# Kernel optimization log

Measured on AMD Instinct MI355X. Metric: run time of the kernel, lower is better.

The kernel has to match this reference:

```python
import jax, jax.numpy as jnp
import numpy as np

BS, T, S_LEN = 128, 256, 40
NV, NS = 2048, 300
VH, SH = 512, 512
L_CROSS, N_LOC, N_FEAT = 512, 128, 1024


def _linear_params(key, out_d, in_d):
    k1, k2 = jax.random.split(key)
    lim = 1.0 / np.sqrt(in_d)
    W = jax.random.uniform(k1, (out_d, in_d), jnp.float32, -lim, lim)
    b = jax.random.uniform(k2, (out_d,), jnp.float32, -lim, lim)
    return W, b


def setup_inputs() -> dict:
    key = jax.random.key(0)
    ks = jax.random.split(key, 12)
    gv = jax.random.normal(ks[0], (BS, T, NV), jnp.float32)
    sen = jax.random.normal(ks[1], (BS, S_LEN, NS), jnp.float32)
    visual_fea = jax.random.normal(ks[2], (BS, T, 2 * VH), jnp.float32)
    sen_fea = jax.random.normal(ks[3], (BS, 2 * SH), jnp.float32)
    loc = jax.random.uniform(ks[4], (BS, 2), jnp.float32)  # normalized start/end in [0,1)
    v_len = jax.random.randint(ks[5], (BS,), 1, T + 1)
    video_mask = (jnp.arange(T)[None, :] < v_len[:, None]).astype(jnp.int32)
    s_len = jax.random.randint(ks[6], (BS,), 1, S_LEN + 1)
    sen_mask = (jnp.arange(S_LEN)[None, :] < s_len[:, None]).astype(jnp.int32)
    W1, b1 = _linear_params(ks[7], L_CROSS, 2 * VH)
    W2, b2 = _linear_params(ks[8], L_CROSS, 2 * SH)
    W3, b3 = _linear_params(ks[9], N_LOC, 2)
    n_cat = 2 * (VH + SH) + L_CROSS + N_LOC
    W4, b4 = _linear_params(ks[10], N_FEAT, n_cat)
    return dict(step=1, gv=gv, sen=sen, visual_fea=visual_fea, sen_fea=sen_fea,
                loc=loc, sen_mask=sen_mask, video_mask=video_mask,
                W1=W1, b1=b1, W2=W2, b2=b2, W3=W3, b3=b3, W4=W4, b4=b4)


def _pool_and_head(visual_fea, sen_fea, loc, video_mask,
                   W1, b1, W2, b2, W3, b3, W4, b4):
    dt = visual_fea.dtype
    n_frame = visual_fea.shape[1]
    v_len = video_mask.sum(1)  # [B] int
    valid = (jnp.arange(n_frame)[None, :] < v_len[:, None]).astype(dt)  # [B,T]
    # global mean over valid frames
    gv_fea = (visual_fea * valid[:, :, None]).sum(1) / v_len[:, None].astype(dt)
    # local mean over [start, end] with start/end = floor(loc * (len-1)) (torch int() trunc, loc>=0)
    idx = jnp.floor(loc * (v_len[:, None] - 1).astype(loc.dtype)).astype(jnp.int32)
    s, e = idx[:, 0], idx[:, 1]
    csum = jnp.cumsum(visual_fea, axis=1)
    csum = jnp.concatenate([jnp.zeros_like(csum[:, :1]), csum], axis=1)  # [B,T+1,D]
    seg_sum = (jnp.take_along_axis(csum, (e + 1)[:, None, None], axis=1)
               - jnp.take_along_axis(csum, s[:, None, None], axis=1))[:, 0, :]
    cnt = jnp.maximum(e + 1 - s, 1).astype(dt)
    lv_fea = jnp.where((s <= e)[:, None], seg_sum / cnt[:, None], jnp.zeros((), dt))
    # fused head
    vs = jax.nn.relu((lv_fea @ W1.T + b1) * (sen_fea @ W2.T + b2))
    loc_fea = jax.nn.relu(loc @ W3.T + b3)
    out = jnp.concatenate([sen_fea, gv_fea, vs, loc_fea], axis=1)
    feature = jax.nn.relu(out @ W4.T + b4)
    return feature


def reference(step, gv, sen, visual_fea, sen_fea, loc, sen_mask, video_mask,
              W1, b1, W2, b2, W3, b3, W4, b4):
    # step != 0 hot path: GRU encodes (step==0 one-time branch) are skipped;
    # visual_fea / sen_fea are carried over from the step-0 call, as in the original.
    assert step != 0, 'reference covers the recurrent hot path (step > 0)'
    feature = _pool_and_head(visual_fea, sen_fea, loc, video_mask,
                             W1, b1, W2, b2, W3, b3, W4, b4)
    return visual_fea, sen_fea, feature
```

## Files before the change

### kernel.cpp

```cpp
#include <hip/hip_runtime.h>

#define BS 128
#define T 256
#define D 1024
#define NCAT 2688
#define NLOC 128
#define NFEAT 1024

typedef short bf16x8 __attribute__((ext_vector_type(8)));
typedef float f32x4 __attribute__((ext_vector_type(4)));
typedef unsigned short u16;
typedef u16 u16x4 __attribute__((ext_vector_type(4)));

__device__ __forceinline__ u16 f2bf(float f) {
    unsigned int u = __float_as_uint(f);
    u += 0x7fffu + ((u >> 16) & 1u);
    return (u16)(u >> 16);
}

__global__ void ka_copy_pool_w(const float* __restrict__ vf, float* __restrict__ out0,
                               const int* __restrict__ vmask, const float* __restrict__ loc,
                               const float* __restrict__ W1, const float* __restrict__ W2,
                               const float* __restrict__ W4,
                               u16* __restrict__ W1b, u16* __restrict__ W2b,
                               u16* __restrict__ W4b,
                               float* __restrict__ pgv, float* __restrict__ pseg) {
    int blk = blockIdx.x, tid = threadIdx.x;

    if (blk >= 1024) {
        int i = (blk - 1024) * 256 + tid;
        const float* src; u16* dst;
        if (i < 131072)      { src = W1 + 4 * i;            dst = W1b + 4 * i; }
        else if (i < 262144) { src = W2 + 4 * (i - 131072); dst = W2b + 4 * (i - 131072); }
        else                 { src = W4 + 4 * (i - 262144); dst = W4b + 4 * (i - 262144); }
        f32x4 v = *(const f32x4*)src;
        u16x4 o;
#pragma unroll
        for (int j = 0; j < 4; ++j) o[j] = f2bf(v[j]);
        *(u16x4*)dst = o;
        return;
    }

    int b = blk >> 3, tc = blk & 7;
    __shared__ int red[256];
    __shared__ int sse[3];
    red[tid] = vmask[b * T + tid];
    __syncthreads();
    for (int off = 128; off > 0; off >>= 1) {
        if (tid < off) red[tid] += red[tid + off];
        __syncthreads();
    }
    if (tid == 0) {
        int vl = red[0];
        float sc = (float)(vl - 1);
        sse[0] = vl;
        sse[1] = (int)floorf(loc[2 * b] * sc);
        sse[2] = (int)floorf(loc[2 * b + 1] * sc);
    }
    __syncthreads();
    int vl = sse[0], s = sse[1], e = sse[2];

    int d0 = tid * 4;
    f32x4 g  = {0.f, 0.f, 0.f, 0.f};
    f32x4 sg = {0.f, 0.f, 0.f, 0.f};
    const float* src = vf   + ((size_t)(b * T + tc * 32)) * D + d0;
    float*       dst = out0 + ((size_t)(b * T + tc * 32)) * D + d0;

    for (int i = 0; i < 32; ++i) {
        f32x4 v = *(const f32x4*)src;
        __builtin_nontemporal_store(v, (f32x4*)dst);
        int t = tc * 32 + i;
        if (t < vl) g += v;
        if (t >= s && t <= e) sg += v;
        src += D; dst += D;
    }
    int o = (b * 8 + tc) * D + d0;
    *(f32x4*)(pgv  + o) = g;
    *(f32x4*)(pseg + o) = sg;
}

__global__ void k2_build(const float* __restrict__ sen_fea, const float* __restrict__ loc,
                         const float* __restrict__ W3, const float* __restrict__ b3,
                         const int* __restrict__ vmask,
                         const float* __restrict__ pgv, const float* __restrict__ pseg,
                         u16* __restrict__ lv_bf, u16* __restrict__ cat,
                         float* __restrict__ out1) {
    int b = blockIdx.x, tid = threadIdx.x;
    __shared__ int red[256];
    __shared__ int sse[3];
    red[tid] = vmask[b * T + tid];
    __syncthreads();
    for (int off = 128; off > 0; off >>= 1) {
        if (tid < off) red[tid] += red[tid + off];
        __syncthreads();
    }
    if (tid == 0) {
        int vl = red[0];
        float sc = (float)(vl - 1);
        sse[0] = vl;
        sse[1] = (int)floorf(loc[2 * b] * sc);
        sse[2] = (int)floorf(loc[2 * b + 1] * sc);
    }
    __syncthreads();
    int vl = sse[0], s = sse[1], e = sse[2];

    float inv_vl = 1.0f / (float)vl;
    int cnt = e + 1 - s; if (cnt < 1) cnt = 1;
    float inv_cnt = 1.0f / (float)cnt;
    bool valid = (s <= e);

    for (int d = tid; d < D; d += 256) {
        float gs = 0.f, ss = 0.f;
#pragma unroll
        for (int c = 0; c < 8; ++c) {
            gs += pgv [(b * 8 + c) * D + d];
            ss += pseg[(b * 8 + c) * D + d];
        }
        cat[b * NCAT + 1024 + d] = f2bf(gs * inv_vl);
        lv_bf[b * D + d] = f2bf(valid ? ss * inv_cnt : 0.f);
        float sf = sen_fea[b * D + d];
        cat[b * NCAT + d] = f2bf(sf);
        out1[b * D + d] = sf;
    }
    if (tid < NLOC) {
        float v = loc[2 * b] * W3[2 * tid] + loc[2 * b + 1] * W3[2 * tid + 1] + b3[tid];
        cat[b * NCAT + 2560 + tid] = f2bf(fmaxf(v, 0.f));
    }
}

__global__ void k3_vs(const u16* __restrict__ lv, const u16* __restrict__ cat_ro,
                      const u16* __restrict__ W1b, const float* __restrict__ b1,
                      const u16* __restrict__ W2b, const float* __restrict__ b2,
                      u16* __restrict__ cat) {
    int wid = threadIdx.x >> 6, lane = threadIdx.x & 63;
    int mt = blockIdx.x >> 5, nt = blockIdx.x & 31;
    int m0 = mt * 16, n0 = nt * 16;
    int row = lane & 15, kg = lane >> 4;

    const u16* pa = (wid == 0) ? (lv + (m0 + row) * D + kg * 8)
                               : (cat_ro + (m0 + row) * NCAT + kg * 8);
    const u16* pb = ((wid == 0) ? W1b : W2b) + (n0 + row) * D + kg * 8;

    f32x4 acc = {0.f, 0.f, 0.f, 0.f};
    for (int k = 0; k < 1024; k += 32)
        acc = __builtin_amdgcn_mfma_f32_16x16x32_bf16(*(const bf16x8*)(pa + k),
                                                      *(const bf16x8*)(pb + k), acc, 0, 0, 0);

    int col = lane & 15, rbase = (lane >> 4) * 4;
    float bb = ((wid == 0) ? b1 : b2)[n0 + col];

    __shared__ float qs[4][64];
    if (wid == 1) {
#pragma unroll
        for (int r = 0; r < 4; ++r) qs[r][lane] = acc[r] + bb;
    }
    __syncthreads();
    if (wid == 0) {
#pragma unroll
        for (int r = 0; r < 4; ++r) {
            float p = acc[r] + bb;
            cat[(m0 + rbase + r) * NCAT + 2048 + n0 + col] = f2bf(fmaxf(p * qs[r][lane], 0.f));
        }
    }
}

__global__ void k4_feat(const u16* __restrict__ cat, const u16* __restrict__ W4b,
                        const float* __restrict__ b4, float* __restrict__ out2) {
    int wid = threadIdx.x >> 6, lane = threadIdx.x & 63;
    int mt = blockIdx.x >> 6, nt = blockIdx.x & 63;
    int m0 = mt * 16, n0 = nt * 16;
    int row = lane & 15, kg = lane >> 4;

    const u16* pa = cat + (m0 + row) * NCAT + wid * 1344 + kg * 8;
    const u16* pb = W4b + (n0 + row) * NCAT + wid * 1344 + kg * 8;

    f32x4 acc = {0.f, 0.f, 0.f, 0.f};
    for (int k = 0; k < 1344; k += 32)
        acc = __builtin_amdgcn_mfma_f32_16x16x32_bf16(*(const bf16x8*)(pa + k),
                                                      *(const bf16x8*)(pb + k), acc, 0, 0, 0);

    int col = lane & 15, rbase = (lane >> 4) * 4;
    __shared__ float qs[4][64];
    if (wid == 1) {
#pragma unroll
        for (int r = 0; r < 4; ++r) qs[r][lane] = acc[r];
    }
    __syncthreads();
    if (wid == 0) {
        float bb = b4[n0 + col];
#pragma unroll
        for (int r = 0; r < 4; ++r)
            out2[(m0 + rbase + r) * NFEAT + n0 + col] = fmaxf(acc[r] + qs[r][lane] + bb, 0.f);
    }
}

extern "C" void kernel_launch(void* const* d_in, const int* in_sizes, int n_in,
                              void* d_out, int out_size, void* d_ws, size_t ws_size,
                              hipStream_t stream) {
    (void)in_sizes; (void)n_in; (void)out_size; (void)ws_size;
    const float* vf      = (const float*)d_in[3];
    const float* sen_fea = (const float*)d_in[4];
    const float* loc     = (const float*)d_in[5];
    const int*   vmask   = (const int*)d_in[7];
    const float* W1 = (const float*)d_in[8];
    const float* b1 = (const float*)d_in[9];
    const float* W2 = (const float*)d_in[10];
    const float* b2 = (const float*)d_in[11];
    const float* W3 = (const float*)d_in[12];
    const float* b3 = (const float*)d_in[13];
    const float* W4 = (const float*)d_in[14];
    const float* b4 = (const float*)d_in[15];

    float* out0 = (float*)d_out;
    float* out1 = out0 + (size_t)BS * T * D;
    float* out2 = out1 + (size_t)BS * D;

    char* w = (char*)d_ws;
    float* pgv  = (float*)(w);
    float* pseg = (float*)(w + 4194304);
    u16*   cat  = (u16*)  (w + 2 * 4194304);
    u16*   lv   = (u16*)  (w + 2 * 4194304 + 688128);
    u16*   W1b  = (u16*)  (w + 2 * 4194304 + 950272);
    u16*   W2b  = (u16*)  (w + 2 * 4194304 + 950272 + 1048576);
    u16*   W4b  = (u16*)  (w + 2 * 4194304 + 950272 + 2097152);

    ka_copy_pool_w<<<4736, 256, 0, stream>>>(vf, out0, vmask, loc, W1, W2, W4,
                                             W1b, W2b, W4b, pgv, pseg);
    k2_build<<<BS, 256, 0, stream>>>(sen_fea, loc, W3, b3, vmask, pgv, pseg, lv, cat, out1);
    k3_vs<<<256, 128, 0, stream>>>(lv, cat, W1b, b1, W2b, b2, cat);
    k4_feat<<<512, 128, 0, stream>>>(cat, W4b, b4, out2);
}
```

Before: 71.08 us.

## Fuse pooling finalize via last-block atomic, defer padded-frame copy to overlap final GEMM

The pool kernel now reads and copies only the valid frames per batch and skips chunks past the video length. The last chunk block to finish, found with an atomic counter, does the reduction and builds the concat buffer, which removes the separate build kernel. Copying the padded frames into the output moves into the final GEMM launch so it runs alongside the MFMA work. The final GEMM also splits K across four waves instead of two. This adds a memset, an atomic counter and cross-block coordination through memory ordering.

```diff
diff --git a/kernel.cpp b/kernel.cpp
--- a/kernel.cpp
+++ b/kernel.cpp
@@ -4,7 +4,6 @@
 #define T 256
 #define D 1024
 #define NCAT 2688
-#define NLOC 128
 #define NFEAT 1024
 
 typedef short bf16x8 __attribute__((ext_vector_type(8)));
@@ -18,13 +17,18 @@
     return (u16)(u >> 16);
 }
 
-__global__ void ka_copy_pool_w(const float* __restrict__ vf, float* __restrict__ out0,
-                               const int* __restrict__ vmask, const float* __restrict__ loc,
-                               const float* __restrict__ W1, const float* __restrict__ W2,
-                               const float* __restrict__ W4,
-                               u16* __restrict__ W1b, u16* __restrict__ W2b,
-                               u16* __restrict__ W4b,
-                               float* __restrict__ pgv, float* __restrict__ pseg) {
+
+__global__ __launch_bounds__(256, 4)
+void kL1(const float* __restrict__ vf, float* __restrict__ out0,
+         const int* __restrict__ vmask, const float* __restrict__ loc,
+         const float* __restrict__ sen_fea,
+         const float* __restrict__ W1, const float* __restrict__ W2,
+         const float* __restrict__ W3, const float* __restrict__ W4,
+         const float* __restrict__ b3,
+         u16* __restrict__ W1b, u16* __restrict__ W2b, u16* __restrict__ W4b,
+         float* __restrict__ pgv, float* __restrict__ pseg,
+         u16* __restrict__ cat, u16* __restrict__ lv,
+         float* __restrict__ out1, int* __restrict__ ctl) {
     int blk = blockIdx.x, tid = threadIdx.x;
 
     if (blk >= 1024) {
@@ -44,6 +48,7 @@
     int b = blk >> 3, tc = blk & 7;
     __shared__ int red[256];
     __shared__ int sse[3];
+    __shared__ int lastf;
     red[tid] = vmask[b * T + tid];
     __syncthreads();
     for (int off = 128; off > 0; off >>= 1) {
@@ -59,73 +64,58 @@
     }
     __syncthreads();
     int vl = sse[0], s = sse[1], e = sse[2];
-
+    int nchunk = (vl + 31) >> 5;
+    if (tc >= nchunk) return;
+
+    int t0 = tc * 32;
+    int nrows = vl - t0; if (nrows > 32) nrows = 32;
     int d0 = tid * 4;
     f32x4 g  = {0.f, 0.f, 0.f, 0.f};
     f32x4 sg = {0.f, 0.f, 0.f, 0.f};
-    const float* src = vf   + ((size_t)(b * T + tc * 32)) * D + d0;
-    float*       dst = out0 + ((size_t)(b * T + tc * 32)) * D + d0;
-
-    for (int i = 0; i < 32; ++i) {
+    const float* src = vf   + ((size_t)(b * T + t0)) * D + d0;
+    float*       dst = out0 + ((size_t)(b * T + t0)) * D + d0;
+    for (int i = 0; i < nrows; ++i) {
         f32x4 v = *(const f32x4*)src;
         __builtin_nontemporal_store(v, (f32x4*)dst);
-        int t = tc * 32 + i;
-        if (t < vl) g += v;
+        g += v;
+        int t = t0 + i;
         if (t >= s && t <= e) sg += v;
         src += D; dst += D;
     }
     int o = (b * 8 + tc) * D + d0;
     *(f32x4*)(pgv  + o) = g;
     *(f32x4*)(pseg + o) = sg;
-}
-
-__global__ void k2_build(const float* __restrict__ sen_fea, const float* __restrict__ loc,
-                         const float* __restrict__ W3, const float* __restrict__ b3,
-                         const int* __restrict__ vmask,
-                         const float* __restrict__ pgv, const float* __restrict__ pseg,
-                         u16* __restrict__ lv_bf, u16* __restrict__ cat,
-                         float* __restrict__ out1) {
-    int b = blockIdx.x, tid = threadIdx.x;
-    __shared__ int red[256];
-    __shared__ int sse[3];
-    red[tid] = vmask[b * T + tid];
-    __syncthreads();
-    for (int off = 128; off > 0; off >>= 1) {
-        if (tid < off) red[tid] += red[tid + off];
-        __syncthreads();
-    }
+
+    __syncthreads();
     if (tid == 0) {
-        int vl = red[0];
-        float sc = (float)(vl - 1);
-        sse[0] = vl;
-        sse[1] = (int)floorf(loc[2 * b] * sc);
-        sse[2] = (int)floorf(loc[2 * b + 1] * sc);
-    }
-    __syncthreads();
-    int vl = sse[0], s = sse[1], e = sse[2];
+        int old = __hip_atomic_fetch_add(&ctl[b], 1,
+                                         __ATOMIC_ACQ_REL, __HIP_MEMORY_SCOPE_AGENT);
+        lastf = (old == nchunk - 1);
+    }
+    __syncthreads();
+    if (!lastf) return;
 
     float inv_vl = 1.0f / (float)vl;
     int cnt = e + 1 - s; if (cnt < 1) cnt = 1;
     float inv_cnt = 1.0f / (float)cnt;
     bool valid = (s <= e);
-
     for (int d = tid; d < D; d += 256) {
         float gs = 0.f, ss = 0.f;
-#pragma unroll
-        for (int c = 0; c < 8; ++c) {
+        for (int c = 0; c < nchunk; ++c) {
             gs += pgv [(b * 8 + c) * D + d];
             ss += pseg[(b * 8 + c) * D + d];
         }
         cat[b * NCAT + 1024 + d] = f2bf(gs * inv_vl);
-        lv_bf[b * D + d] = f2bf(valid ? ss * inv_cnt : 0.f);
+        lv[b * D + d] = f2bf(valid ? ss * inv_cnt : 0.f);
         float sf = sen_fea[b * D + d];
         cat[b * NCAT + d] = f2bf(sf);
         out1[b * D + d] = sf;
     }
-    if (tid < NLOC) {
+    if (tid < 128) {
         float v = loc[2 * b] * W3[2 * tid] + loc[2 * b + 1] * W3[2 * tid + 1] + b3[tid];
         cat[b * NCAT + 2560 + tid] = f2bf(fmaxf(v, 0.f));
     }
+    if (tid == 0) ctl[128 + b] = vl;
 }
 
 __global__ void k3_vs(const u16* __restrict__ lv, const u16* __restrict__ cat_ro,
@@ -164,33 +154,59 @@
     }
 }
 
-__global__ void k4_feat(const u16* __restrict__ cat, const u16* __restrict__ W4b,
-                        const float* __restrict__ b4, float* __restrict__ out2) {
-    int wid = threadIdx.x >> 6, lane = threadIdx.x & 63;
-    int mt = blockIdx.x >> 6, nt = blockIdx.x & 63;
-    int m0 = mt * 16, n0 = nt * 16;
-    int row = lane & 15, kg = lane >> 4;
-
-    const u16* pa = cat + (m0 + row) * NCAT + wid * 1344 + kg * 8;
-    const u16* pb = W4b + (n0 + row) * NCAT + wid * 1344 + kg * 8;
-
-    f32x4 acc = {0.f, 0.f, 0.f, 0.f};
-    for (int k = 0; k < 1344; k += 32)
-        acc = __builtin_amdgcn_mfma_f32_16x16x32_bf16(*(const bf16x8*)(pa + k),
-                                                      *(const bf16x8*)(pb + k), acc, 0, 0, 0);
-
-    int col = lane & 15, rbase = (lane >> 4) * 4;
-    __shared__ float qs[4][64];
-    if (wid == 1) {
-#pragma unroll
-        for (int r = 0; r < 4; ++r) qs[r][lane] = acc[r];
-    }
-    __syncthreads();
-    if (wid == 0) {
-        float bb = b4[n0 + col];
-#pragma unroll
-        for (int r = 0; r < 4; ++r)
-            out2[(m0 + rbase + r) * NFEAT + n0 + col] = fmaxf(acc[r] + qs[r][lane] + bb, 0.f);
+__global__ __launch_bounds__(256, 4)
+void kL3(const float* __restrict__ vf, float* __restrict__ out0,
+         const u16* __restrict__ cat, const u16* __restrict__ W4b,
+         const float* __restrict__ b4, float* __restrict__ out2,
+         const int* __restrict__ ctl) {
+    int blk = blockIdx.x, tid = threadIdx.x;
+    __shared__ float qsf[3][4][64];
+
+    if (blk < 512) {
+        int mt = blk >> 6, nt = blk & 63;
+        int wid = tid >> 6, lane = tid & 63;
+        int m0 = mt * 16, n0 = nt * 16;
+        int row = lane & 15, kg = lane >> 4;
+
+        const u16* pa = cat + (m0 + row) * NCAT + wid * 672 + kg * 8;
+        const u16* pb = W4b + (n0 + row) * NCAT + wid * 672 + kg * 8;
+
+        f32x4 acc = {0.f, 0.f, 0.f, 0.f};
+        for (int k = 0; k < 672; k += 32)
+            acc = __builtin_amdgcn_mfma_f32_16x16x32_bf16(*(const bf16x8*)(pa + k),
+                                                          *(const bf16x8*)(pb + k), acc, 0, 0, 0);
+        int col = lane & 15, rbase = (lane >> 4) * 4;
+        if (wid) {
+#pragma unroll
+            for (int r = 0; r < 4; ++r) qsf[wid - 1][r][lane] = acc[r];
+        }
+        __syncthreads();
+        if (wid == 0) {
+            float bb = b4[n0 + col];
+#pragma unroll
+            for (int r = 0; r < 4; ++r) {
+                float v = acc[r] + qsf[0][r][lane] + qsf[1][r][lane] + qsf[2][r][lane] + bb;
+                out2[(m0 + rbase + r) * NFEAT + n0 + col] = fmaxf(v, 0.f);
+            }
+        }
+        return;
+    }
+
+    int bi = blk - 512;
+    int b = bi >> 3, tc = bi & 7;
+    int vl = ctl[128 + b];
+    int t0 = tc * 32;
+    int start = (vl > t0) ? vl : t0;
+    int end = t0 + 32;
+    if (start >= end) return;
+
+    int d0 = tid * 4;
+    const float* src = vf   + ((size_t)(b * T + start)) * D + d0;
+    float*       dst = out0 + ((size_t)(b * T + start)) * D + d0;
+    for (int t = start; t < end; ++t) {
+        f32x4 v = *(const f32x4*)src;
+        __builtin_nontemporal_store(v, (f32x4*)dst);
+        src += D; dst += D;
     }
 }
 
@@ -216,17 +232,19 @@
     float* out2 = out1 + (size_t)BS * D;
 
     char* w = (char*)d_ws;
-    float* pgv  = (float*)(w);
-    float* pseg = (float*)(w + 4194304);
-    u16*   cat  = (u16*)  (w + 2 * 4194304);
-    u16*   lv   = (u16*)  (w + 2 * 4194304 + 688128);
-    u16*   W1b  = (u16*)  (w + 2 * 4194304 + 950272);
-    u16*   W2b  = (u16*)  (w + 2 * 4194304 + 950272 + 1048576);
-    u16*   W4b  = (u16*)  (w + 2 * 4194304 + 950272 + 2097152);
-
-    ka_copy_pool_w<<<4736, 256, 0, stream>>>(vf, out0, vmask, loc, W1, W2, W4,
-                                             W1b, W2b, W4b, pgv, pseg);
-    k2_build<<<BS, 256, 0, stream>>>(sen_fea, loc, W3, b3, vmask, pgv, pseg, lv, cat, out1);
+    int*   ctl  = (int*)w;
+    float* pgv  = (float*)(w + 4096);
+    float* pseg = (float*)(w + 4096 + 4194304);
+    u16*   cat  = (u16*)  (w + 4096 + 2 * 4194304);
+    u16*   lv   = (u16*)  (w + 4096 + 2 * 4194304 + 688128);
+    u16*   W1b  = (u16*)  (w + 4096 + 2 * 4194304 + 950272);
+    u16*   W2b  = (u16*)  (w + 4096 + 2 * 4194304 + 950272 + 1048576);
+    u16*   W4b  = (u16*)  (w + 4096 + 2 * 4194304 + 950272 + 2097152);
+
+    hipMemsetAsync(ctl, 0, 512, stream);
+    kL1<<<4736, 256, 0, stream>>>(vf, out0, vmask, loc, sen_fea,
+                                  W1, W2, W3, W4, b3,
+                                  W1b, W2b, W4b, pgv, pseg, cat, lv, out1, ctl);
     k3_vs<<<256, 128, 0, stream>>>(lv, cat, W1b, b1, W2b, b2, cat);
-    k4_feat<<<512, 128, 0, stream>>>(cat, W4b, b4, out2);
-}
+    kL3<<<1536, 256, 0, stream>>>(vf, out0, cat, W4b, b4, out2, ctl);
+}
```

After: 132.6 us. 86.5% more time.

## Move half of the visual_fea copy into the final GEMM kernel and split K across four waves

Applied to the files above, without the earlier changes.

The first kernel now writes only the first half of the time steps of out0 while still reading everything for pooling. The second half of the passthrough copy is done by extra blocks appended to the final W4 GEMM kernel, so that bandwidth-bound copy work can overlap with the small, latency-bound GEMM. The GEMM now splits K across four waves instead of two and reduces the partials through shared memory. The cost is that the second half of visual_fea is read twice, adding extra global read traffic.

```diff
diff --git a/kernel.cpp b/kernel.cpp
--- a/kernel.cpp
+++ b/kernel.cpp
@@ -4,7 +4,6 @@
 #define T 256
 #define D 1024
 #define NCAT 2688
-#define NLOC 128
 #define NFEAT 1024
 
 typedef short bf16x8 __attribute__((ext_vector_type(8)));
@@ -18,13 +17,13 @@
     return (u16)(u >> 16);
 }
 
-__global__ void ka_copy_pool_w(const float* __restrict__ vf, float* __restrict__ out0,
-                               const int* __restrict__ vmask, const float* __restrict__ loc,
-                               const float* __restrict__ W1, const float* __restrict__ W2,
-                               const float* __restrict__ W4,
-                               u16* __restrict__ W1b, u16* __restrict__ W2b,
-                               u16* __restrict__ W4b,
-                               float* __restrict__ pgv, float* __restrict__ pseg) {
+__global__ __launch_bounds__(256, 4)
+void ka(const float* __restrict__ vf, float* __restrict__ out0,
+        const int* __restrict__ vmask, const float* __restrict__ loc,
+        const float* __restrict__ W1, const float* __restrict__ W2,
+        const float* __restrict__ W4,
+        u16* __restrict__ W1b, u16* __restrict__ W2b, u16* __restrict__ W4b,
+        float* __restrict__ pgv, float* __restrict__ pseg) {
     int blk = blockIdx.x, tid = threadIdx.x;
 
     if (blk >= 1024) {
@@ -60,19 +59,30 @@
     __syncthreads();
     int vl = sse[0], s = sse[1], e = sse[2];
 
+    int t0 = tc * 32;
     int d0 = tid * 4;
     f32x4 g  = {0.f, 0.f, 0.f, 0.f};
     f32x4 sg = {0.f, 0.f, 0.f, 0.f};
-    const float* src = vf   + ((size_t)(b * T + tc * 32)) * D + d0;
-    float*       dst = out0 + ((size_t)(b * T + tc * 32)) * D + d0;
-
-    for (int i = 0; i < 32; ++i) {
-        f32x4 v = *(const f32x4*)src;
-        __builtin_nontemporal_store(v, (f32x4*)dst);
-        int t = tc * 32 + i;
-        if (t < vl) g += v;
-        if (t >= s && t <= e) sg += v;
-        src += D; dst += D;
+    const float* src = vf   + ((size_t)(b * T + t0)) * D + d0;
+    float*       dst = out0 + ((size_t)(b * T + t0)) * D + d0;
+
+    if (tc < 4) {
+        for (int i = 0; i < 32; ++i) {
+            f32x4 v = *(const f32x4*)src;
+            __builtin_nontemporal_store(v, (f32x4*)dst);
+            int t = t0 + i;
+            if (t < vl) g += v;
+            if (t >= s && t <= e) sg += v;
+            src += D; dst += D;
+        }
+    } else {
+        for (int i = 0; i < 32; ++i) {
+            f32x4 v = *(const f32x4*)src;
+            int t = t0 + i;
+            if (t < vl) g += v;
+            if (t >= s && t <= e) sg += v;
+            src += D;
+        }
     }
     int o = (b * 8 + tc) * D + d0;
     *(f32x4*)(pgv  + o) = g;
@@ -122,7 +132,7 @@
         cat[b * NCAT + d] = f2bf(sf);
         out1[b * D + d] = sf;
     }
-    if (tid < NLOC) {
+    if (tid < 128) {
         float v = loc[2 * b] * W3[2 * tid] + loc[2 * b + 1] * W3[2 * tid + 1] + b3[tid];
         cat[b * NCAT + 2560 + tid] = f2bf(fmaxf(v, 0.f));
     }
@@ -164,33 +174,53 @@
     }
 }
 
-__global__ void k4_feat(const u16* __restrict__ cat, const u16* __restrict__ W4b,
-                        const float* __restrict__ b4, float* __restrict__ out2) {
-    int wid = threadIdx.x >> 6, lane = threadIdx.x & 63;
-    int mt = blockIdx.x >> 6, nt = blockIdx.x & 63;
+__global__ __launch_bounds__(256, 4)
+void kD(const float* __restrict__ vf, float* __restrict__ out0,
+        const u16* __restrict__ cat, const u16* __restrict__ W4b,
+        const float* __restrict__ b4, float* __restrict__ out2) {
+    int blk = blockIdx.x, tid = threadIdx.x;
+    __shared__ float qsf[3][4][64];
+
+    if (blk >= 512) {
+        int ci = blk - 512;
+        int b = ci >> 2, tc = 4 + (ci & 3);
+        int t0 = tc * 32;
+        int d0 = tid * 4;
+        const float* src = vf   + ((size_t)(b * T + t0)) * D + d0;
+        float*       dst = out0 + ((size_t)(b * T + t0)) * D + d0;
+        for (int i = 0; i < 32; ++i) {
+            f32x4 v = *(const f32x4*)src;
+            __builtin_nontemporal_store(v, (f32x4*)dst);
+            src += D; dst += D;
+        }
+        return;
+    }
+
+    int mt = blk >> 6, nt = blk & 63;
+    int wid = tid >> 6, lane = tid & 63;
     int m0 = mt * 16, n0 = nt * 16;
     int row = lane & 15, kg = lane >> 4;
 
-    const u16* pa = cat + (m0 + row) * NCAT + wid * 1344 + kg * 8;
-    const u16* pb = W4b + (n0 + row) * NCAT + wid * 1344 + kg * 8;
+    const u16* pa = cat + (m0 + row) * NCAT + wid * 672 + kg * 8;
+    const u16* pb = W4b + (n0 + row) * NCAT + wid * 672 + kg * 8;
 
     f32x4 acc = {0.f, 0.f, 0.f, 0.f};
-    for (int k = 0; k < 1344; k += 32)
+    for (int k = 0; k < 672; k += 32)
         acc = __builtin_amdgcn_mfma_f32_16x16x32_bf16(*(const bf16x8*)(pa + k),
                                                       *(const bf16x8*)(pb + k), acc, 0, 0, 0);
-
     int col = lane & 15, rbase = (lane >> 4) * 4;
-    __shared__ float qs[4][64];
-    if (wid == 1) {
-#pragma unroll
-        for (int r = 0; r < 4; ++r) qs[r][lane] = acc[r];
+    if (wid) {
+#pragma unroll
+        for (int r = 0; r < 4; ++r) qsf[wid - 1][r][lane] = acc[r];
     }
     __syncthreads();
     if (wid == 0) {
         float bb = b4[n0 + col];
 #pragma unroll
-        for (int r = 0; r < 4; ++r)
-            out2[(m0 + rbase + r) * NFEAT + n0 + col] = fmaxf(acc[r] + qs[r][lane] + bb, 0.f);
+        for (int r = 0; r < 4; ++r) {
+            float v = acc[r] + qsf[0][r][lane] + qsf[1][r][lane] + qsf[2][r][lane] + bb;
+            out2[(m0 + rbase + r) * NFEAT + n0 + col] = fmaxf(v, 0.f);
+        }
     }
 }
 
@@ -224,9 +254,9 @@
     u16*   W2b  = (u16*)  (w + 2 * 4194304 + 950272 + 1048576);
     u16*   W4b  = (u16*)  (w + 2 * 4194304 + 950272 + 2097152);
 
-    ka_copy_pool_w<<<4736, 256, 0, stream>>>(vf, out0, vmask, loc, W1, W2, W4,
-                                             W1b, W2b, W4b, pgv, pseg);
+    ka<<<4736, 256, 0, stream>>>(vf, out0, vmask, loc, W1, W2, W4,
+                                 W1b, W2b, W4b, pgv, pseg);
     k2_build<<<BS, 256, 0, stream>>>(sen_fea, loc, W3, b3, vmask, pgv, pseg, lv, cat, out1);
     k3_vs<<<256, 128, 0, stream>>>(lv, cat, W1b, b1, W2b, b2, cat);
-    k4_feat<<<512, 128, 0, stream>>>(cat, W4b, b4, out2);
-}
+    kD<<<1024, 256, 0, stream>>>(vf, out0, cat, W4b, b4, out2);
+}
```

New measurement: 89.03 us. 25.2% more time.
